# Kernel optimization log

Measured on AMD Instinct MI355X. Metric: run time of the kernel, lower is better.

Reference implementation:

```python
import jax, jax.numpy as jnp
import numpy as np

B, N, D = 2, 128, 128          # batch, nodes, dim
DE = 64                        # dim_edge_refinement
H, DH = 8, 32                  # heads, per-head dim
DI = H * DH                    # dim_inner = dim * dim_head = 256
DMI = 2 * DI                   # mlp_expansion_factor * dim_inner = 512
MD = 2                         # max_degree
S = 1 + 2 * MD                 # value/edge channel groups = 5
FFD = 512                      # int(2.0 * dim * 2) for EquivariantFeedForward


def _ln(x, g, eps=1e-5):
    mu = x.mean(-1, keepdims=True)
    var = ((x - mu) ** 2).mean(-1, keepdims=True)
    return (x - mu) / jnp.sqrt(var + eps) * g


def setup_inputs() -> dict:
    key = jax.random.key(0)
    ks = iter(jax.random.split(key, 64))
    def rn(shape, scale=1.0):
        return jax.random.normal(next(ks), shape, dtype=jnp.float32) * scale
    w = 0.05
    return dict(
        h=rn((B, N, D)), x1=rn((B, N, D, 3)), x2=rn((B, N, D, 5)),
        t_ij=rn((B, N, N, D)), r1=rn((B, N, N, 3)), r2=rn((B, N, N, 5)),
        g_i=jnp.ones((D,), jnp.float32), g_j=jnp.ones((D,), jnp.float32),
        Wq=rn((D, DI), w), Wk=rn((D, DI), w),
        Wv1=rn((D, DMI), w), bv1=jnp.zeros((DMI,), jnp.float32),
        Wv2=rn((DMI, S * DI), w), bv2=jnp.zeros((S * DI,), jnp.float32),
        Wp1=rn((D, DMI), w), bp1=jnp.zeros((DMI,), jnp.float32),
        Wp2=rn((DMI, S * DI), w), bp2=jnp.zeros((S * DI,), jnp.float32),
        Wek=rn((D, S * DI), w), Wev=rn((D, S * DI), w),
        Wcomb=rn((DI, D), w),
        Wqh=rn((D, DE), w), Wk1h=rn((D, DE), w), Wk2h=rn((D, DE), w),
        Wep=rn((2 * DE, D), w), Wres=rn((D, D), w),
        P1=rn((D, D), w), P2=rn((D, D), w),
        Wf1a=rn((2 * D, FFD), w), bf1a=jnp.zeros((FFD,), jnp.float32),
        Wf2a=rn((FFD, 2 * D), w), bf2a=jnp.zeros((2 * D,), jnp.float32),
        Wf1b=rn((2 * D, FFD), w), bf1b=jnp.zeros((FFD,), jnp.float32),
        Wf2b=rn((FFD, 2 * D), w), bf2b=jnp.zeros((2 * D,), jnp.float32),
    )


def reference(h, x1, x2, t_ij, r1, r2, g_i, g_j, Wq, Wk, Wv1, bv1, Wv2, bv2,
              Wp1, bp1, Wp2, bp2, Wek, Wev, Wcomb, Wqh, Wk1h, Wk2h, Wep, Wres,
              P1, P2, Wf1a, bf1a, Wf2a, bf2a, Wf1b, bf1b, Wf2b, bf2b):
    # ---- HierarchicalTensorRefinement: per-degree inner products -> edge refresh
    q1 = jnp.einsum('bndm,de->bnem', x1, Wqh)
    q2 = jnp.einsum('bndm,de->bnem', x2, Wqh)
    k1 = jnp.einsum('bndm,de->bnem', x1, Wk1h)
    k2 = jnp.einsum('bndm,de->bnem', x2, Wk2h)
    w_ij = jnp.concatenate([
        jnp.einsum('biem,bjem->bije', q1, k1),
        jnp.einsum('biem,bjem->bije', q2, k2)], axis=-1)       # [b,n,n,2*DE]
    t = w_ij @ Wep + t_ij @ Wres                                # [b,n,n,D]
    # ---- GeometryAwareTensorAttention
    hi = _ln(h, g_i)
    hj = _ln(h, g_j)
    q = (hi @ Wq).reshape(B, N, H, DH).transpose(0, 2, 1, 3)    # bhnd
    k = (hj @ Wk).reshape(B, N, H, DH).transpose(0, 2, 1, 3)
    v = (jax.nn.silu(hj @ Wv1 + bv1) @ Wv2 + bv2).reshape(B, N, S, H, DH).transpose(0, 3, 1, 2, 4)   # bhnsd
    pv = (jax.nn.silu(hj @ Wp1 + bp1) @ Wp2 + bp2).reshape(B, N, S, H, DH).transpose(0, 3, 1, 2, 4)
    ek = jax.nn.silu(t @ Wek).reshape(B, N, N, S, H, DH).transpose(0, 4, 1, 2, 3, 5)                  # bhijsd
    ev = (t @ Wev).reshape(B, N, N, S, H, DH).transpose(0, 4, 1, 2, 3, 5)
    sim_num = jnp.einsum('bhid,bhjd->bhij', q, k)
    sim_den = jnp.einsum('bhid,bhijsd->bhis', q, ek)            # edge-keyed denominator
    attn = sim_num[..., None] / sim_den[:, :, :, None, :]       # bhijs
    sea = attn[..., None] * v[:, :, None] + ev * pv[:, :, None]  # bhijsd
    out = sea.transpose(0, 2, 3, 4, 1, 5).reshape(B, N, N, S, H * DH) @ Wcomb  # [b,i,j,S,D]
    h_sc = out[..., 0, :]              # [b,i,j,D]
    r_sc = out[..., 1:1 + MD, :]       # [b,i,j,MD,D]
    x_sc = out[..., 1 + MD:, :]        # [b,i,j,MD,D]
    h2 = h + h_sc.sum(axis=2)
    x1a = jnp.einsum('bjdm,bijd->bidm', x1, x_sc[..., 0, :]) + jnp.einsum('bijm,bijd->bidm', r1, r_sc[..., 0, :])
    x2a = jnp.einsum('bjdm,bijd->bidm', x2, x_sc[..., 1, :]) + jnp.einsum('bijm,bijd->bidm', r2, r_sc[..., 1, :])
    # ---- EquivariantFeedForward (eq 13)
    def ff_branch(xl, P, W1, b1, W2, b2):
        proj = jnp.einsum('bndm,de->bnem', xl, P)
        inv = jnp.sqrt((proj ** 2).sum(-1) + 1e-12)             # invariant norm over m
        mo = jax.nn.silu(jnp.concatenate([h2, inv], -1) @ W1 + b1) @ W2 + b2
        m1, m2 = jnp.split(mo, 2, axis=-1)
        return m1, proj * m2[..., None]
    m1a, xr1 = ff_branch(x1a, P1, Wf1a, bf1a, Wf2a, bf2a)
    m1b, xr2 = ff_branch(x2a, P2, Wf1b, bf1b, Wf2b, bf2b)
    h3 = h2 + m1a + m1b
    x1f = x1a + xr1
    x2f = x2a + xr2
    # pack outputs: h [b,n,d,1] | x1 [b,n,d,3] | x2 [b,n,d,5] -> [b,n,d,9]
    return jnp.concatenate([h3[..., None], x1f, x2f], axis=-1)
```

## Files before the change

### kernel.cpp

```cpp
#include <hip/hip_runtime.h>
#include <math.h>

#define OFF_Q    0
#define OFF_K    65536
#define OFF_A1V  131072
#define OFF_A1P  262144
#define OFF_V    393216
#define OFF_PV   720896
#define OFF_VW   1048576
#define OFF_QK   2359296
#define OFF_T    2621440
#define OFF_DEN  6815744
#define OFF_ACC  6825984
#define OFF_WEVT 7940096
#define OFF_WCT  8022016
#define OFF_HI   8038400
#define OFF_HJ   8071168

typedef __bf16 bf16x8 __attribute__((ext_vector_type(8)));
typedef float  f32x4  __attribute__((ext_vector_type(4)));

__device__ __forceinline__ float silu_f(float x){
  return x / (1.0f + __expf(-x));
}
__device__ __forceinline__ unsigned short f2bf(float x){
  union{float f; unsigned u;} c; c.f = x;
  unsigned r = c.u + 0x7FFFu + ((c.u >> 16) & 1u);
  return (unsigned short)(r >> 16);
}
__device__ __forceinline__ unsigned packbf(float a, float b){
  return (unsigned)f2bf(a) | ((unsigned)f2bf(b) << 16);
}
__device__ __forceinline__ void swz_store(float* Abase, int k, int j, float v){
  *(float*)((char*)Abase + k*256 + ((((j>>2) ^ ((k>>2)&15))) << 4) + ((j&3)<<2)) = v;
}
__device__ __forceinline__ f32x4 swz_load4(const float* Abase, int k, int chunk){
  return *(const f32x4*)((const char*)Abase + k*256 + ((chunk ^ ((k>>2)&15)) << 4));
}

__global__ __launch_bounds__(128) void k0a_ln(
    const float* __restrict__ h, const float* __restrict__ g_i, const float* __restrict__ g_j,
    float* __restrict__ ws)
{
  __shared__ float red[2];
  const int r = blockIdx.x, tid = threadIdx.x;
  const int w = tid >> 6, l = tid & 63;
  const float hv = h[r*128 + tid];
  float s = hv;
  #pragma unroll
  for (int o = 1; o < 64; o <<= 1) s += __shfl_xor(s, o);
  if (l == 0) red[w] = s;
  __syncthreads();
  const float mu = (red[0] + red[1]) * (1.f/128.f);
  const float dv = hv - mu;
  float s2 = dv*dv;
  #pragma unroll
  for (int o = 1; o < 64; o <<= 1) s2 += __shfl_xor(s2, o);
  __syncthreads();
  if (l == 0) red[w] = s2;
  __syncthreads();
  const float rstd = 1.0f / sqrtf((red[0] + red[1])*(1.f/128.f) + 1e-5f);
  ws[OFF_HI + r*128 + tid] = dv * rstd * g_i[tid];
  ws[OFF_HJ + r*128 + tid] = dv * rstd * g_j[tid];
  if (tid < 40) ws[OFF_DEN + r*40 + tid] = 0.f;
}

__global__ __launch_bounds__(256) void k0b_qkv(
    const float* __restrict__ Wq, const float* __restrict__ Wk,
    const float* __restrict__ Wv1, const float* __restrict__ bv1,
    const float* __restrict__ Wp1, const float* __restrict__ bp1,
    float* __restrict__ ws)
{
  __shared__ float hrow[128];
  const int bid = blockIdx.x;
  const int row = bid / 6, ch = bid - 6*(bid/6);
  const int tid = threadIdx.x;
  if (tid < 128) hrow[tid] = ws[((ch == 0) ? OFF_HI : OFF_HJ) + row*128 + tid];
  __syncthreads();
  const float* W; int c; float bias = 0.f; bool act = false; float* dst; int wstride;
  switch(ch){
    case 0: W = Wq;  c = tid;      wstride = 256; dst = ws + OFF_Q   + row*256 + c; break;
    case 1: W = Wk;  c = tid;      wstride = 256; dst = ws + OFF_K   + row*256 + c; break;
    case 2: W = Wv1; c = tid;      wstride = 512; bias = bv1[c]; act = true; dst = ws + OFF_A1V + row*512 + c; break;
    case 3: W = Wv1; c = 256+tid;  wstride = 512; bias = bv1[c]; act = true; dst = ws + OFF_A1V + row*512 + c; break;
    case 4: W = Wp1; c = tid;      wstride = 512; bias = bp1[c]; act = true; dst = ws + OFF_A1P + row*512 + c; break;
    default:W = Wp1; c = 256+tid;  wstride = 512; bias = bp1[c]; act = true; dst = ws + OFF_A1P + row*512 + c; break;
  }
  float acc = bias;
  #pragma unroll 8
  for (int d = 0; d < 128; ++d) acc += hrow[d] * W[d*wstride + c];
  *dst = act ? silu_f(acc) : acc;
}

__global__ __launch_bounds__(256) void k0c_qk12(
    const float* __restrict__ x1, const float* __restrict__ x2,
    const float* __restrict__ Wqh, const float* __restrict__ Wk1h, const float* __restrict__ Wk2h,
    float* __restrict__ ws)
{
  __shared__ float x1r[384], x2r[640];
  const int row = blockIdx.x, tid = threadIdx.x;
  for (int idx = tid; idx < 384; idx += 256) x1r[idx] = x1[row*384 + idx];
  for (int idx = tid; idx < 640; idx += 256) x2r[idx] = x2[row*640 + idx];
  __syncthreads();
  for (int idx = tid; idx < 512; idx += 256){
    if (idx < 192){
      const int e = idx/3, m = idx - e*3;
      float qa = 0.f, ka = 0.f;
      #pragma unroll 8
      for (int d = 0; d < 128; ++d){
        const float xv = x1r[d*3 + m];
        qa += xv*Wqh[d*64 + e];
        ka += xv*Wk1h[d*64 + e];
      }
      ws[OFF_QK + row*1024 + idx] = qa;
      ws[OFF_QK + row*1024 + 512 + idx] = ka;
    } else {
      const int i2 = idx - 192;
      const int e = i2/5, m = i2 - e*5;
      float qa = 0.f, ka = 0.f;
      #pragma unroll 8
      for (int d = 0; d < 128; ++d){
        const float xv = x2r[d*5 + m];
        qa += xv*Wqh[d*64 + e];
        ka += xv*Wk2h[d*64 + e];
      }
      ws[OFF_QK + row*1024 + 192 + i2] = qa;
      ws[OFF_QK + row*1024 + 704 + i2] = ka;
    }
  }
}

__global__ __launch_bounds__(256) void k1_vp(
    const float* __restrict__ Wv2, const float* __restrict__ bv2,
    const float* __restrict__ Wp2, const float* __restrict__ bp2,
    float* __restrict__ ws)
{
  __shared__ float A[512][16];
  __shared__ float Bc[64][128];
  const int tid = threadIdx.x;
  const int rt = blockIdx.x & 31;
  const int ct = blockIdx.x >> 5;
  const int r0 = rt*16;
  const bool isP = (r0 >= 256);
  const int rbase = isP ? (r0 - 256) : r0;
  const float* __restrict__ src  = ws + (isP ? OFF_A1P : OFF_A1V);
  const float* __restrict__ W    = isP ? Wp2 : Wv2;
  const float* __restrict__ bias = isP ? bp2 : bv2;
  const int c0 = ct*128;
  for (int idx = tid; idx < 2048; idx += 256){
    const int rl = idx & 15;
    const int c4 = (idx >> 4) * 4;
    const float4 v = *(const float4*)&src[(rbase+rl)*512 + c4];
    A[c4+0][rl] = v.x; A[c4+1][rl] = v.y; A[c4+2][rl] = v.z; A[c4+3][rl] = v.w;
  }
  float acc[4][2] = {{0.f}};
  const int rg = tid & 3;
  const int cg = tid >> 2;
  for (int kc = 0; kc < 8; ++kc){
    __syncthreads();
    for (int idx = tid; idx < 2048; idx += 256){
      const int kl = idx >> 5;
      const int c4 = (idx & 31)*4;
      *(float4*)&Bc[kl][c4] = *(const float4*)&W[(kc*64+kl)*1280 + c0 + c4];
    }
    __syncthreads();
    #pragma unroll 8
    for (int k = 0; k < 64; ++k){
      const float4 a = *(const float4*)&A[kc*64+k][rg*4];
      const float b0 = Bc[k][cg*2], b1 = Bc[k][cg*2+1];
      acc[0][0] += a.x*b0; acc[0][1] += a.x*b1;
      acc[1][0] += a.y*b0; acc[1][1] += a.y*b1;
      acc[2][0] += a.z*b0; acc[2][1] += a.z*b1;
      acc[3][0] += a.w*b0; acc[3][1] += a.w*b1;
    }
  }
  float* __restrict__ dst = ws + (isP ? OFF_PV : OFF_V);
  for (int rr = 0; rr < 4; ++rr)
    for (int cc = 0; cc < 2; ++cc){
      const int c = c0 + cg*2 + cc;
      dst[(rbase + rg*4 + rr)*1280 + c] = acc[rr][cc] + bias[c];
    }
}

__global__ __launch_bounds__(256) void k2_vw(const float* __restrict__ Wcomb, float* __restrict__ ws)
{
  __shared__ float vr[1280];
  const int j = blockIdx.x, tid = threadIdx.x;
  for (int idx = tid; idx < 320; idx += 256)
    *(float4*)&vr[idx*4] = *(const float4*)&ws[OFF_V + j*1280 + idx*4];
  __syncthreads();
  const int d = tid & 127;
  for (int sh = tid >> 7; sh < 40; sh += 2){
    const int s = sh >> 3, hh = sh & 7;
    float a = 0.f;
    #pragma unroll 8
    for (int dh = 0; dh < 32; ++dh)
      a += vr[s*256 + hh*32 + dh] * Wcomb[(hh*32+dh)*128 + d];
    ws[OFF_VW + j*5120 + sh*128 + d] = a;
  }
}

__global__ __launch_bounds__(256) void k_cvt(
    const float* __restrict__ Wev, const float* __restrict__ Wcomb, float* __restrict__ ws)
{
  __shared__ float ld[16][256];
  const int tid = threadIdx.x;
  if (blockIdx.x < 80){
    const int c0 = blockIdx.x*16;
    for (int p = 0; p < 8; ++p){
      const int idx = tid + p*256;
      const int k = idx >> 4, cl = idx & 15;
      ld[cl][k] = Wev[k*1280 + c0 + cl];
    }
    __syncthreads();
    const int cl = tid >> 4, k8 = tid & 15;
    uint4 u;
    u.x = packbf(ld[cl][k8*8+0], ld[cl][k8*8+1]);
    u.y = packbf(ld[cl][k8*8+2], ld[cl][k8*8+3]);
    u.z = packbf(ld[cl][k8*8+4], ld[cl][k8*8+5]);
    u.w = packbf(ld[cl][k8*8+6], ld[cl][k8*8+7]);
    ((uint4*)(ws + OFF_WEVT))[(c0+cl)*16 + k8] = u;
  } else {
    const int c0 = (blockIdx.x - 80)*16;
    for (int p = 0; p < 16; ++p){
      const int idx = tid + p*256;
      const int k = idx >> 4, cl = idx & 15;
      ld[cl][k] = Wcomb[k*128 + c0 + cl];
    }
    __syncthreads();
    const int cl = tid >> 4, k8i = tid & 15;
    for (int pass = 0; pass < 2; ++pass){
      const int k8 = k8i + pass*16;
      uint4 u;
      u.x = packbf(ld[cl][k8*8+0], ld[cl][k8*8+1]);
      u.y = packbf(ld[cl][k8*8+2], ld[cl][k8*8+3]);
      u.z = packbf(ld[cl][k8*8+4], ld[cl][k8*8+5]);
      u.w = packbf(ld[cl][k8*8+6], ld[cl][k8*8+7]);
      ((uint4*)(ws + OFF_WCT))[(c0+cl)*32 + k8] = u;
    }
  }
}

__global__ __launch_bounds__(512, 2) void k3_t(
    const float* __restrict__ t_ij, const float* __restrict__ Wep, const float* __restrict__ Wres,
    float* __restrict__ ws)
{
  __shared__ float A[16384];
  __shared__ float qrow[512];
  float* kst = A + 8192;
  const int tid = threadIdx.x;
  const int bi = blockIdx.x >> 1;
  const int jt = blockIdx.x & 1;
  const int j0 = jt*64;
  const int b  = bi >> 7;
  if (tid < 128) *(float4*)&qrow[tid*4] = *(const float4*)&ws[OFF_QK + bi*1024 + tid*4];
  for (int jq = 0; jq < 4; ++jq){
    __syncthreads();
    for (int idx = tid; idx < 2048; idx += 512){
      const int jl = idx & 15;
      const int c4 = (idx >> 4)*4;
      const float4 v = *(const float4*)&ws[OFF_QK + (b*128 + j0 + jq*16 + jl)*1024 + 512 + c4];
      kst[(c4+0)*16 + jl] = v.x; kst[(c4+1)*16 + jl] = v.y;
      kst[(c4+2)*16 + jl] = v.z; kst[(c4+3)*16 + jl] = v.w;
    }
    __syncthreads();
    for (int idx = tid; idx < 2048; idx += 512){
      const int jl = idx & 15;
      const int e  = idx >> 4;
      float acc = 0.f;
      if (e < 64){
        #pragma unroll
        for (int m = 0; m < 3; ++m) acc += qrow[e*3+m] * kst[(e*3+m)*16 + jl];
      } else {
        const int e2 = e - 64;
        #pragma unroll
        for (int m = 0; m < 5; ++m) acc += qrow[192 + e2*5+m] * kst[(192 + e2*5+m)*16 + jl];
      }
      swz_store(A, e, jq*16 + jl, acc);
    }
  }
  __syncthreads();
  for (int idx = tid; idx < 2048; idx += 512){
    const int jl = idx >> 5;
    const int d4 = (idx & 31)*4;
    const float4 v = *(const float4*)&t_ij[(bi*128 + j0 + jl)*128 + d4];
    swz_store(A, 128+d4+0, jl, v.x);
    swz_store(A, 128+d4+1, jl, v.y);
    swz_store(A, 128+d4+2, jl, v.z);
    swz_store(A, 128+d4+3, jl, v.w);
  }
  __syncthreads();
  const int jg = tid >> 5;
  const int cg = tid & 31;
  f32x4 acc[4] = {{0,0,0,0},{0,0,0,0},{0,0,0,0},{0,0,0,0}};
  {
    const float* Wp = Wep + cg*4;
    f32x4 wv = *(const f32x4*)Wp;
    for (int k = 0; k < 127; ++k){
      const f32x4 wn = *(const f32x4*)(Wp + (k+1)*128);
      const f32x4 av = swz_load4(A, k, jg);
      acc[0] += wv*av[0]; acc[1] += wv*av[1]; acc[2] += wv*av[2]; acc[3] += wv*av[3];
      wv = wn;
    }
    const f32x4 av = swz_load4(A, 127, jg);
    acc[0] += wv*av[0]; acc[1] += wv*av[1]; acc[2] += wv*av[2]; acc[3] += wv*av[3];
  }
  {
    const float* Wp = Wres + cg*4;
    f32x4 wv = *(const f32x4*)Wp;
    for (int k = 0; k < 127; ++k){
      const f32x4 wn = *(const f32x4*)(Wp + (k+1)*128);
      const f32x4 av = swz_load4(A, 128+k, jg);
      acc[0] += wv*av[0]; acc[1] += wv*av[1]; acc[2] += wv*av[2]; acc[3] += wv*av[3];
      wv = wn;
    }
    const f32x4 av = swz_load4(A, 255, jg);
    acc[0] += wv*av[0]; acc[1] += wv*av[1]; acc[2] += wv*av[2]; acc[3] += wv*av[3];
  }
  #pragma unroll
  for (int jj = 0; jj < 4; ++jj)
    *(f32x4*)&ws[OFF_T + (bi*128 + j0 + jg*4 + jj)*128 + cg*4] = acc[jj];
}

__global__ __launch_bounds__(256) void k4_den(
    const float* __restrict__ Wek, float* __restrict__ ws)
{
  __shared__ float tl[8192];
  __shared__ float colsum[8][128];
  __shared__ float den40[40];
  const int tid = threadIdx.x;
  const int bid = blockIdx.x;
  const int bi = bid / 20;
  const int rem = bid - bi*20;
  const int jh = rem & 1;
  const int cq = rem >> 1;
  const int j0 = jh*64;
  for (int idx = tid; idx < 2048; idx += 256){
    const int j = idx >> 5;
    const int d4 = (idx & 31)*4;
    const float4 v = *(const float4*)&ws[OFF_T + (bi*128 + j0 + j)*128 + d4];
    swz_store(tl, d4+0, j, v.x);
    swz_store(tl, d4+1, j, v.y);
    swz_store(tl, d4+2, j, v.z);
    swz_store(tl, d4+3, j, v.w);
  }
  if (tid < 40) den40[tid] = 0.f;
  __syncthreads();
  const int w = tid >> 5;
  const int lane = tid & 31;
  const float* wekp = Wek + cq*128 + lane*4;
  f32x4 acc[8];
  #pragma unroll
  for (int i = 0; i < 8; ++i) acc[i] = (f32x4){0,0,0,0};
  f32x4 wv = *(const f32x4*)wekp;
  for (int k = 0; k < 127; ++k){
    const f32x4 wn = *(const f32x4*)(wekp + (k+1)*1280);
    #pragma unroll
    for (int q = 0; q < 2; ++q){
      const f32x4 tv = swz_load4(tl, k, w*2 + q);
      acc[q*4+0] += wv*tv[0]; acc[q*4+1] += wv*tv[1];
      acc[q*4+2] += wv*tv[2]; acc[q*4+3] += wv*tv[3];
    }
    wv = wn;
  }
  #pragma unroll
  for (int q = 0; q < 2; ++q){
    const f32x4 tv = swz_load4(tl, 127, w*2 + q);
    acc[q*4+0] += wv*tv[0]; acc[q*4+1] += wv*tv[1];
    acc[q*4+2] += wv*tv[2]; acc[q*4+3] += wv*tv[3];
  }
  f32x4 cs = {0,0,0,0};
  #pragma unroll
  for (int i = 0; i < 8; ++i){
    #pragma unroll
    for (int cc = 0; cc < 4; ++cc) cs[cc] += silu_f(acc[i][cc]);
  }
  *(f32x4*)&colsum[w][lane*4] = cs;
  __syncthreads();
  if (tid < 128){
    const int c = tid;
    const float jsum = colsum[0][c] + colsum[1][c] + colsum[2][c] + colsum[3][c]
                     + colsum[4][c] + colsum[5][c] + colsum[6][c] + colsum[7][c];
    const int col = cq*128 + c;
    const int s  = col >> 8;
    const int hd = col & 255;
    atomicAdd(&den40[(hd>>5)*5 + s], jsum * ws[OFF_Q + bi*256 + hd]);
  }
  __syncthreads();
  if (tid < 40 && den40[tid] != 0.f)
    atomicAdd(&ws[OFF_DEN + bi*40 + tid], den40[tid]);
}

__global__ __launch_bounds__(512) void k5_pass2(
    const float* __restrict__ x1, const float* __restrict__ x2,
    const float* __restrict__ r1, const float* __restrict__ r2,
    float* __restrict__ ws)
{
  __shared__ unsigned short epB[2][4096];
  __shared__ float num[8][64];
  __shared__ float acc17[17*128];
  __shared__ float ql[256];
  __shared__ float rdenl[40];

  const int tid  = threadIdx.x;
  const int lane = tid & 63;
  const int w    = tid >> 6;
  const int wm   = w & 3;
  const int wn   = w >> 2;
  const int l15  = lane & 15;
  const int kq   = lane >> 4;

  const int bi = blockIdx.x >> 1;
  const int jh = blockIdx.x & 1;
  const int j0 = jh*64;
  const int b  = bi >> 7;

  if (tid < 64) *(float4*)&ql[tid*4] = *(const float4*)&ws[OFF_Q + bi*256 + tid*4];
  if (tid < 40) rdenl[tid] = 1.0f / ws[OFF_DEN + bi*40 + tid];
  for (int idx = tid; idx < 17*128; idx += 512) acc17[idx] = 0.f;

  const int jA = wm*16 + l15;
  union { bf16x8 v; uint4 q; } afu[4];
  #pragma unroll
  for (int ks = 0; ks < 4; ++ks){
    const float* tp = &ws[OFF_T + (bi*128 + j0 + jA)*128 + ks*32 + kq*8];
    const float4 t0 = *(const float4*)tp;
    const float4 t1 = *(const float4*)(tp + 4);
    afu[ks].q.x = packbf(t0.x, t0.y);
    afu[ks].q.y = packbf(t0.z, t0.w);
    afu[ks].q.z = packbf(t1.x, t1.y);
    afu[ks].q.w = packbf(t1.z, t1.w);
  }
  __syncthreads();

  {
    const int hh = tid >> 6, jl = tid & 63;
    const float* krow = &ws[OFF_K + (b*128 + j0 + jl)*256 + hh*32];
    float a = 0.f;
    #pragma unroll
    for (int dh = 0; dh < 32; ++dh) a += ql[hh*32+dh]*krow[dh];
    num[hh][jl] = a;
  }

  const __bf16* wevt = (const __bf16*)(ws + OFF_WEVT);
  const __bf16* wct  = (const __bf16*)(ws + OFF_WCT);

  int pb = 0;
  for (int s = 0; s < 5; ++s){
    f32x4 o0 = {0,0,0,0}, o1 = {0,0,0,0}, o2 = {0,0,0,0}, o3 = {0,0,0,0};
    for (int ch4 = 0; ch4 < 4; ++ch4){
      const int cb = s*256 + ch4*64;
      f32x4 ev0 = {0,0,0,0}, ev1 = {0,0,0,0};
      {
        const int c0l = wn*32 + l15;
        const int c1l = c0l + 16;
        #pragma unroll
        for (int ks = 0; ks < 4; ++ks){
          const bf16x8 b0 = *(const bf16x8*)(wevt + (cb + c0l)*128 + ks*32 + kq*8);
          const bf16x8 b1 = *(const bf16x8*)(wevt + (cb + c1l)*128 + ks*32 + kq*8);
          ev0 = __builtin_amdgcn_mfma_f32_16x16x32_bf16(afu[ks].v, b0, ev0, 0, 0, 0);
          ev1 = __builtin_amdgcn_mfma_f32_16x16x32_bf16(afu[ks].v, b1, ev1, 0, 0, 0);
        }
      }
      #pragma unroll
      for (int nt = 0; nt < 2; ++nt){
        const int cl = wn*32 + nt*16 + l15;
        const int cglob = cb + cl;
        #pragma unroll
        for (int r = 0; r < 4; ++r){
          const int jl = wm*16 + kq*4 + r;
          const float pvv = ws[OFF_PV + (b*128 + j0 + jl)*1280 + cglob];
          const float evv = (nt == 0) ? ev0[r] : ev1[r];
          *(unsigned short*)((char*)epB[pb] + jl*128 + ((cl*2) ^ ((jl&7)<<4))) = f2bf(evv * pvv);
        }
      }
      __syncthreads();
      #pragma unroll
      for (int ks = 0; ks < 2; ++ks){
        const bf16x8 a = *(const bf16x8*)((const char*)epB[pb] + jA*128 + ((ks*64 + kq*16) ^ ((jA&7)<<4)));
        #pragma unroll
        for (int nt = 0; nt < 4; ++nt){
          const int dl = wn*64 + nt*16 + l15;
          const bf16x8 bb = *(const bf16x8*)(wct + dl*256 + ch4*64 + ks*32 + kq*8);
          if      (nt == 0) o0 = __builtin_amdgcn_mfma_f32_16x16x32_bf16(a, bb, o0, 0, 0, 0);
          else if (nt == 1) o1 = __builtin_amdgcn_mfma_f32_16x16x32_bf16(a, bb, o1, 0, 0, 0);
          else if (nt == 2) o2 = __builtin_amdgcn_mfma_f32_16x16x32_bf16(a, bb, o2, 0, 0, 0);
          else              o3 = __builtin_amdgcn_mfma_f32_16x16x32_bf16(a, bb, o3, 0, 0, 0);
        }
      }
      pb ^= 1;
    }
    #pragma unroll
    for (int r = 0; r < 4; ++r){
      const int jl = wm*16 + kq*4 + r;
      const float* vwbase = ws + OFF_VW + (b*128 + j0 + jl)*5120 + s*1024 + wn*64 + l15;
      #pragma unroll
      for (int hh = 0; hh < 8; ++hh){
        const float at = num[hh][jl] * rdenl[hh*5 + s];
        const float* vp = vwbase + hh*128;
        o0[r] += at * vp[0];
        o1[r] += at * vp[16];
        o2[r] += at * vp[32];
        o3[r] += at * vp[48];
      }
    }
    if (s == 0){
      #pragma unroll
      for (int nt = 0; nt < 4; ++nt){
        const f32x4 oo = (nt==0)?o0:(nt==1)?o1:(nt==2)?o2:o3;
        float p = oo[0] + oo[1] + oo[2] + oo[3];
        p += __shfl_xor(p, 16);
        p += __shfl_xor(p, 32);
        if (lane < 16) atomicAdd(&acc17[wn*64 + nt*16 + lane], p);
      }
    } else if (s <= 2){
      const int M = (s == 1) ? 3 : 5;
      const int slot0 = (s == 1) ? 1 : 4;
      const float* rw = (s == 1) ? r1 : r2;
      for (int m = 0; m < M; ++m){
        float wj[4];
        #pragma unroll
        for (int r = 0; r < 4; ++r)
          wj[r] = rw[(bi*128 + j0 + wm*16 + kq*4 + r)*M + m];
        #pragma unroll
        for (int nt = 0; nt < 4; ++nt){
          const f32x4 oo = (nt==0)?o0:(nt==1)?o1:(nt==2)?o2:o3;
          float p = wj[0]*oo[0] + wj[1]*oo[1] + wj[2]*oo[2] + wj[3]*oo[3];
          p += __shfl_xor(p, 16);
          p += __shfl_xor(p, 32);
          if (lane < 16) atomicAdd(&acc17[(slot0+m)*128 + wn*64 + nt*16 + lane], p);
        }
      }
    } else {
      const int M = (s == 3) ? 3 : 5;
      const int slot0 = (s == 3) ? 9 : 12;
      const float* xw = (s == 3) ? x1 : x2;
      for (int m = 0; m < M; ++m){
        #pragma unroll
        for (int nt = 0; nt < 4; ++nt){
          const int d = wn*64 + nt*16 + l15;
          const f32x4 oo = (nt==0)?o0:(nt==1)?o1:(nt==2)?o2:o3;
          float p = 0.f;
          #pragma unroll
          for (int r = 0; r < 4; ++r)
            p += xw[((b*128 + j0 + wm*16 + kq*4 + r)*128 + d)*M + m] * oo[r];
          p += __shfl_xor(p, 16);
          p += __shfl_xor(p, 32);
          if (lane < 16) atomicAdd(&acc17[(slot0+m)*128 + d], p);
        }
      }
    }
  }
  __syncthreads();
  for (int idx = tid; idx < 2176; idx += 512)
    ws[OFF_ACC + (bi*2 + jh)*2176 + idx] = acc17[idx];
}

__global__ __launch_bounds__(256) void k6_tail(
    const float* __restrict__ h,
    const float* __restrict__ P1, const float* __restrict__ P2,
    const float* __restrict__ Wf1a, const float* __restrict__ bf1a,
    const float* __restrict__ Wf2a, const float* __restrict__ bf2a,
    const float* __restrict__ Wf1b, const float* __restrict__ bf1b,
    const float* __restrict__ Wf2b, const float* __restrict__ bf2b,
    const float* __restrict__ ws, float* __restrict__ out)
{
  __shared__ float a17[2176];
  __shared__ float h2s[128];
  __shared__ float x1a[384], x2a[640];
  __shared__ float pj1[384], pj2[640];
  __shared__ float inv1[128], inv2[128];
  __shared__ float za[512], zb[512];
  __shared__ float m1a[128], m2a[128], m1b[128], m2b[128];
  const int tid = threadIdx.x;
  const int row = blockIdx.x;
  for (int idx = tid; idx < 2176; idx += 256)
    a17[idx] = ws[OFF_ACC + (row*2)*2176 + idx] + ws[OFF_ACC + (row*2+1)*2176 + idx];
  __syncthreads();
  if (tid < 128) h2s[tid] = h[row*128 + tid] + a17[tid];
  for (int idx = tid; idx < 384; idx += 256){
    const int d = idx/3, m = idx - d*3;
    x1a[idx] = a17[(1+m)*128 + d] + a17[(9+m)*128 + d];
  }
  for (int idx = tid; idx < 640; idx += 256){
    const int d = idx/5, m = idx - d*5;
    x2a[idx] = a17[(4+m)*128 + d] + a17[(12+m)*128 + d];
  }
  __syncthreads();
  if (tid < 128){
    const int e = tid;
    float pa[3] = {0.f,0.f,0.f};
    for (int d = 0; d < 128; ++d){
      const float p = P1[d*128 + e];
      pa[0] += x1a[d*3+0]*p;
      pa[1] += x1a[d*3+1]*p;
      pa[2] += x1a[d*3+2]*p;
    }
    pj1[e*3+0] = pa[0]; pj1[e*3+1] = pa[1]; pj1[e*3+2] = pa[2];
    inv1[e] = sqrtf(pa[0]*pa[0] + pa[1]*pa[1] + pa[2]*pa[2] + 1e-12f);
  } else {
    const int e = tid - 128;
    float pa[5] = {0.f,0.f,0.f,0.f,0.f};
    for (int d = 0; d < 128; ++d){
      const float p = P2[d*128 + e];
      pa[0] += x2a[d*5+0]*p;
      pa[1] += x2a[d*5+1]*p;
      pa[2] += x2a[d*5+2]*p;
      pa[3] += x2a[d*5+3]*p;
      pa[4] += x2a[d*5+4]*p;
    }
    #pragma unroll
    for (int m = 0; m < 5; ++m) pj2[e*5+m] = pa[m];
    inv2[e] = sqrtf(pa[0]*pa[0]+pa[1]*pa[1]+pa[2]*pa[2]+pa[3]*pa[3]+pa[4]*pa[4] + 1e-12f);
  }
  __syncthreads();
  for (int it = 0; it < 2; ++it){
    const int f = tid + it*256;
    float av = bf1a[f], bv_ = bf1b[f];
    #pragma unroll 4
    for (int k = 0; k < 128; ++k){
      av  += h2s[k]*Wf1a[k*512 + f];
      bv_ += h2s[k]*Wf1b[k*512 + f];
    }
    #pragma unroll 4
    for (int k = 0; k < 128; ++k){
      av  += inv1[k]*Wf1a[(128+k)*512 + f];
      bv_ += inv2[k]*Wf1b[(128+k)*512 + f];
    }
    za[f] = silu_f(av); zb[f] = silu_f(bv_);
  }
  __syncthreads();
  {
    const int g = tid;
    float am = bf2a[g], bm = bf2b[g];
    #pragma unroll 4
    for (int f = 0; f < 512; ++f){
      am += za[f]*Wf2a[f*256 + g];
      bm += zb[f]*Wf2b[f*256 + g];
    }
    if (g < 128){ m1a[g] = am; m1b[g] = bm; }
    else        { m2a[g-128] = am; m2b[g-128] = bm; }
  }
  __syncthreads();
  if (tid < 128){
    const int d = tid;
    const int ob = (row*128 + d)*9;
    out[ob+0] = h2s[d] + m1a[d] + m1b[d];
    #pragma unroll
    for (int m = 0; m < 3; ++m)
      out[ob+1+m] = x1a[d*3+m] + pj1[d*3+m]*m2a[d];
    #pragma unroll
    for (int m = 0; m < 5; ++m)
      out[ob+4+m] = x2a[d*5+m] + pj2[d*5+m]*m2b[d];
  }
}

extern "C" void kernel_launch(void* const* d_in, const int* in_sizes, int n_in,
                              void* d_out, int out_size, void* d_ws, size_t ws_size,
                              hipStream_t stream)
{
  (void)in_sizes; (void)n_in; (void)out_size; (void)ws_size;
  const float* h    = (const float*)d_in[0];
  const float* x1   = (const float*)d_in[1];
  const float* x2   = (const float*)d_in[2];
  const float* t_ij = (const float*)d_in[3];
  const float* r1   = (const float*)d_in[4];
  const float* r2   = (const float*)d_in[5];
  const float* g_i  = (const float*)d_in[6];
  const float* g_j  = (const float*)d_in[7];
  const float* Wq   = (const float*)d_in[8];
  const float* Wk   = (const float*)d_in[9];
  const float* Wv1  = (const float*)d_in[10];
  const float* bv1  = (const float*)d_in[11];
  const float* Wv2  = (const float*)d_in[12];
  const float* bv2  = (const float*)d_in[13];
  const float* Wp1  = (const float*)d_in[14];
  const float* bp1  = (const float*)d_in[15];
  const float* Wp2  = (const float*)d_in[16];
  const float* bp2  = (const float*)d_in[17];
  const float* Wek  = (const float*)d_in[18];
  const float* Wev  = (const float*)d_in[19];
  const float* Wcomb= (const float*)d_in[20];
  const float* Wqh  = (const float*)d_in[21];
  const float* Wk1h = (const float*)d_in[22];
  const float* Wk2h = (const float*)d_in[23];
  const float* Wep  = (const float*)d_in[24];
  const float* Wres = (const float*)d_in[25];
  const float* P1   = (const float*)d_in[26];
  const float* P2   = (const float*)d_in[27];
  const float* Wf1a = (const float*)d_in[28];
  const float* bf1a = (const float*)d_in[29];
  const float* Wf2a = (const float*)d_in[30];
  const float* bf2a = (const float*)d_in[31];
  const float* Wf1b = (const float*)d_in[32];
  const float* bf1b = (const float*)d_in[33];
  const float* Wf2b = (const float*)d_in[34];
  const float* bf2b = (const float*)d_in[35];
  float* ws  = (float*)d_ws;
  float* out = (float*)d_out;

  k0a_ln <<<dim3(256),  dim3(128), 0, stream>>>(h, g_i, g_j, ws);
  k0b_qkv<<<dim3(1536), dim3(256), 0, stream>>>(Wq, Wk, Wv1, bv1, Wp1, bp1, ws);
  k0c_qk12<<<dim3(256), dim3(256), 0, stream>>>(x1, x2, Wqh, Wk1h, Wk2h, ws);
  k1_vp  <<<dim3(320),  dim3(256), 0, stream>>>(Wv2, bv2, Wp2, bp2, ws);
  k2_vw  <<<dim3(256),  dim3(256), 0, stream>>>(Wcomb, ws);
  k_cvt  <<<dim3(88),   dim3(256), 0, stream>>>(Wev, Wcomb, ws);
  k3_t   <<<dim3(512),  dim3(512), 0, stream>>>(t_ij, Wep, Wres, ws);
  k4_den <<<dim3(5120), dim3(256), 0, stream>>>(Wek, ws);
  k5_pass2<<<dim3(512), dim3(512), 0, stream>>>(x1, x2, r1, r2, ws);
  k6_tail<<<dim3(256),  dim3(256), 0, stream>>>(h, P1, P2, Wf1a, bf1a, Wf2a, bf2a, Wf1b, bf1b, Wf2b, bf2b, ws, out);
}
```

Measured before the change: 717.5 us.

## Split k5_pass2 across channel groups into separate blocks for more parallelism

The k5 pass now launches one block per (row, j-half, channel group s) with 256 threads, instead of one 512-thread block looping over all five groups. Each wave owns 16 rows and all 128 output columns, so it holds eight MFMA accumulators instead of four. This raises the block count fivefold to fill the GPU better and shrinks shared memory to only the slots for one group. In exchange, each block redoes the T-tile bf16 conversion and the q·k numerator, and per-thread register pressure goes up.

```diff
diff --git a/kernel.cpp b/kernel.cpp
--- a/kernel.cpp
+++ b/kernel.cpp
@@ -391,35 +391,39 @@
     atomicAdd(&ws[OFF_DEN + bi*40 + tid], den40[tid]);
 }
 
-__global__ __launch_bounds__(512) void k5_pass2(
+__global__ __launch_bounds__(256) void k5_pass2(
     const float* __restrict__ x1, const float* __restrict__ x2,
     const float* __restrict__ r1, const float* __restrict__ r2,
     float* __restrict__ ws)
 {
   __shared__ unsigned short epB[2][4096];
   __shared__ float num[8][64];
-  __shared__ float acc17[17*128];
+  __shared__ float accS[5*128];
   __shared__ float ql[256];
-  __shared__ float rdenl[40];
+  __shared__ float rden8[8];
 
   const int tid  = threadIdx.x;
   const int lane = tid & 63;
   const int w    = tid >> 6;
-  const int wm   = w & 3;
-  const int wn   = w >> 2;
   const int l15  = lane & 15;
   const int kq   = lane >> 4;
 
-  const int bi = blockIdx.x >> 1;
-  const int jh = blockIdx.x & 1;
-  const int j0 = jh*64;
-  const int b  = bi >> 7;
-
-  if (tid < 64) *(float4*)&ql[tid*4] = *(const float4*)&ws[OFF_Q + bi*256 + tid*4];
-  if (tid < 40) rdenl[tid] = 1.0f / ws[OFF_DEN + bi*40 + tid];
-  for (int idx = tid; idx < 17*128; idx += 512) acc17[idx] = 0.f;
-
-  const int jA = wm*16 + l15;
+  const int bid = blockIdx.x;
+  const int bi  = bid / 10;
+  const int rem = bid - bi*10;
+  const int jh  = rem & 1;
+  const int s   = rem >> 1;
+  const int j0  = jh*64;
+  const int b   = bi >> 7;
+
+  const int M     = (s == 0) ? 1 : ((s == 1 || s == 3) ? 3 : 5);
+  const int slot0 = (s == 0) ? 0 : (s == 1) ? 1 : (s == 2) ? 4 : (s == 3) ? 9 : 12;
+
+  ql[tid] = ws[OFF_Q + bi*256 + tid];
+  if (tid < 8) rden8[tid] = 1.0f / ws[OFF_DEN + bi*40 + tid*5 + s];
+  for (int idx = tid; idx < M*128; idx += 256) accS[idx] = 0.f;
+
+  const int jA = w*16 + l15;
   union { bf16x8 v; uint4 q; } afu[4];
   #pragma unroll
   for (int ks = 0; ks < 4; ++ks){
@@ -433,8 +437,8 @@
   }
   __syncthreads();
 
-  {
-    const int hh = tid >> 6, jl = tid & 63;
+  for (int idx = tid; idx < 512; idx += 256){
+    const int hh = idx >> 6, jl = idx & 63;
     const float* krow = &ws[OFF_K + (b*128 + j0 + jl)*256 + hh*32];
     float a = 0.f;
     #pragma unroll
@@ -445,115 +449,120 @@
   const __bf16* wevt = (const __bf16*)(ws + OFF_WEVT);
   const __bf16* wct  = (const __bf16*)(ws + OFF_WCT);
 
+  f32x4 o0={0,0,0,0},o1={0,0,0,0},o2={0,0,0,0},o3={0,0,0,0},
+        o4={0,0,0,0},o5={0,0,0,0},o6={0,0,0,0},o7={0,0,0,0};
   int pb = 0;
-  for (int s = 0; s < 5; ++s){
-    f32x4 o0 = {0,0,0,0}, o1 = {0,0,0,0}, o2 = {0,0,0,0}, o3 = {0,0,0,0};
-    for (int ch4 = 0; ch4 < 4; ++ch4){
-      const int cb = s*256 + ch4*64;
-      f32x4 ev0 = {0,0,0,0}, ev1 = {0,0,0,0};
-      {
-        const int c0l = wn*32 + l15;
-        const int c1l = c0l + 16;
-        #pragma unroll
-        for (int ks = 0; ks < 4; ++ks){
-          const bf16x8 b0 = *(const bf16x8*)(wevt + (cb + c0l)*128 + ks*32 + kq*8);
-          const bf16x8 b1 = *(const bf16x8*)(wevt + (cb + c1l)*128 + ks*32 + kq*8);
-          ev0 = __builtin_amdgcn_mfma_f32_16x16x32_bf16(afu[ks].v, b0, ev0, 0, 0, 0);
-          ev1 = __builtin_amdgcn_mfma_f32_16x16x32_bf16(afu[ks].v, b1, ev1, 0, 0, 0);
-        }
+  for (int ch4 = 0; ch4 < 4; ++ch4){
+    const int cb = s*256 + ch4*64;
+    f32x4 ev0={0,0,0,0},ev1={0,0,0,0},ev2={0,0,0,0},ev3={0,0,0,0};
+    #pragma unroll
+    for (int ks = 0; ks < 4; ++ks){
+      const __bf16* bp = wevt + (cb + l15)*128 + ks*32 + kq*8;
+      const bf16x8 b0 = *(const bf16x8*)(bp);
+      const bf16x8 b1 = *(const bf16x8*)(bp + 16*128);
+      const bf16x8 b2 = *(const bf16x8*)(bp + 32*128);
+      const bf16x8 b3 = *(const bf16x8*)(bp + 48*128);
+      ev0 = __builtin_amdgcn_mfma_f32_16x16x32_bf16(afu[ks].v, b0, ev0, 0, 0, 0);
+      ev1 = __builtin_amdgcn_mfma_f32_16x16x32_bf16(afu[ks].v, b1, ev1, 0, 0, 0);
+      ev2 = __builtin_amdgcn_mfma_f32_16x16x32_bf16(afu[ks].v, b2, ev2, 0, 0, 0);
+      ev3 = __builtin_amdgcn_mfma_f32_16x16x32_bf16(afu[ks].v, b3, ev3, 0, 0, 0);
+    }
+    #pragma unroll
+    for (int nt = 0; nt < 4; ++nt){
+      const int cl = nt*16 + l15;
+      const int cglob = cb + cl;
+      const f32x4 evv = (nt==0)?ev0:(nt==1)?ev1:(nt==2)?ev2:ev3;
+      #pragma unroll
+      for (int r = 0; r < 4; ++r){
+        const int jl = w*16 + kq*4 + r;
+        const float pvv = ws[OFF_PV + (b*128 + j0 + jl)*1280 + cglob];
+        *(unsigned short*)((char*)epB[pb] + jl*128 + ((cl*2) ^ ((jl&7)<<4))) = f2bf(evv[r] * pvv);
       }
+    }
+    __syncthreads();
+    #pragma unroll
+    for (int ks = 0; ks < 2; ++ks){
+      const bf16x8 a = *(const bf16x8*)((const char*)epB[pb] + jA*128 + ((ks*64 + kq*16) ^ ((jA&7)<<4)));
       #pragma unroll
-      for (int nt = 0; nt < 2; ++nt){
-        const int cl = wn*32 + nt*16 + l15;
-        const int cglob = cb + cl;
-        #pragma unroll
-        for (int r = 0; r < 4; ++r){
-          const int jl = wm*16 + kq*4 + r;
-          const float pvv = ws[OFF_PV + (b*128 + j0 + jl)*1280 + cglob];
-          const float evv = (nt == 0) ? ev0[r] : ev1[r];
-          *(unsigned short*)((char*)epB[pb] + jl*128 + ((cl*2) ^ ((jl&7)<<4))) = f2bf(evv * pvv);
-        }
+      for (int nt = 0; nt < 8; ++nt){
+        const int dl = nt*16 + l15;
+        const bf16x8 bb = *(const bf16x8*)(wct + dl*256 + ch4*64 + ks*32 + kq*8);
+        if      (nt == 0) o0 = __builtin_amdgcn_mfma_f32_16x16x32_bf16(a, bb, o0, 0, 0, 0);
+        else if (nt == 1) o1 = __builtin_amdgcn_mfma_f32_16x16x32_bf16(a, bb, o1, 0, 0, 0);
+        else if (nt == 2) o2 = __builtin_amdgcn_mfma_f32_16x16x32_bf16(a, bb, o2, 0, 0, 0);
+        else if (nt == 3) o3 = __builtin_amdgcn_mfma_f32_16x16x32_bf16(a, bb, o3, 0, 0, 0);
+        else if (nt == 4) o4 = __builtin_amdgcn_mfma_f32_16x16x32_bf16(a, bb, o4, 0, 0, 0);
+        else if (nt == 5) o5 = __builtin_amdgcn_mfma_f32_16x16x32_bf16(a, bb, o5, 0, 0, 0);
+        else if (nt == 6) o6 = __builtin_amdgcn_mfma_f32_16x16x32_bf16(a, bb, o6, 0, 0, 0);
+        else              o7 = __builtin_amdgcn_mfma_f32_16x16x32_bf16(a, bb, o7, 0, 0, 0);
       }
-      __syncthreads();
+    }
+    pb ^= 1;
+  }
+  #pragma unroll
+  for (int r = 0; r < 4; ++r){
+    const int jl = w*16 + kq*4 + r;
+    const float* vwbase = ws + OFF_VW + (b*128 + j0 + jl)*5120 + s*1024 + l15;
+    #pragma unroll
+    for (int hh = 0; hh < 8; ++hh){
+      const float at = num[hh][jl] * rden8[hh];
+      const float* vp = vwbase + hh*128;
+      o0[r] += at * vp[0];
+      o1[r] += at * vp[16];
+      o2[r] += at * vp[32];
+      o3[r] += at * vp[48];
+      o4[r] += at * vp[64];
+      o5[r] += at * vp[80];
+      o6[r] += at * vp[96];
+      o7[r] += at * vp[112];
+    }
+  }
+  if (s == 0){
+    #pragma unroll
+    for (int nt = 0; nt < 8; ++nt){
+      const f32x4 oo = (nt==0)?o0:(nt==1)?o1:(nt==2)?o2:(nt==3)?o3:(nt==4)?o4:(nt==5)?o5:(nt==6)?o6:o7;
+      float p = oo[0] + oo[1] + oo[2] + oo[3];
+      p += __shfl_xor(p, 16);
+      p += __shfl_xor(p, 32);
+      if (l15 == lane) ;
+      if (lane < 16) atomicAdd(&accS[nt*16 + lane], p);
+    }
+  } else if (s <= 2){
+    const float* rw = (s == 1) ? r1 : r2;
+    for (int m = 0; m < M; ++m){
+      float wj[4];
       #pragma unroll
-      for (int ks = 0; ks < 2; ++ks){
-        const bf16x8 a = *(const bf16x8*)((const char*)epB[pb] + jA*128 + ((ks*64 + kq*16) ^ ((jA&7)<<4)));
-        #pragma unroll
-        for (int nt = 0; nt < 4; ++nt){
-          const int dl = wn*64 + nt*16 + l15;
-          const bf16x8 bb = *(const bf16x8*)(wct + dl*256 + ch4*64 + ks*32 + kq*8);
-          if      (nt == 0) o0 = __builtin_amdgcn_mfma_f32_16x16x32_bf16(a, bb, o0, 0, 0, 0);
-          else if (nt == 1) o1 = __builtin_amdgcn_mfma_f32_16x16x32_bf16(a, bb, o1, 0, 0, 0);
-          else if (nt == 2) o2 = __builtin_amdgcn_mfma_f32_16x16x32_bf16(a, bb, o2, 0, 0, 0);
-          else              o3 = __builtin_amdgcn_mfma_f32_16x16x32_bf16(a, bb, o3, 0, 0, 0);
-        }
-      }
-      pb ^= 1;
-    }
-    #pragma unroll
-    for (int r = 0; r < 4; ++r){
-      const int jl = wm*16 + kq*4 + r;
-      const float* vwbase = ws + OFF_VW + (b*128 + j0 + jl)*5120 + s*1024 + wn*64 + l15;
+      for (int r = 0; r < 4; ++r)
+        wj[r] = rw[(bi*128 + j0 + w*16 + kq*4 + r)*M + m];
       #pragma unroll
-      for (int hh = 0; hh < 8; ++hh){
-        const float at = num[hh][jl] * rdenl[hh*5 + s];
-        const float* vp = vwbase + hh*128;
-        o0[r] += at * vp[0];
-        o1[r] += at * vp[16];
-        o2[r] += at * vp[32];
-        o3[r] += at * vp[48];
-      }
-    }
-    if (s == 0){
-      #pragma unroll
-      for (int nt = 0; nt < 4; ++nt){
-        const f32x4 oo = (nt==0)?o0:(nt==1)?o1:(nt==2)?o2:o3;
-        float p = oo[0] + oo[1] + oo[2] + oo[3];
+      for (int nt = 0; nt < 8; ++nt){
+        const f32x4 oo = (nt==0)?o0:(nt==1)?o1:(nt==2)?o2:(nt==3)?o3:(nt==4)?o4:(nt==5)?o5:(nt==6)?o6:o7;
+        float p = wj[0]*oo[0] + wj[1]*oo[1] + wj[2]*oo[2] + wj[3]*oo[3];
         p += __shfl_xor(p, 16);
         p += __shfl_xor(p, 32);
-        if (lane < 16) atomicAdd(&acc17[wn*64 + nt*16 + lane], p);
+        if (lane < 16) atomicAdd(&accS[m*128 + nt*16 + lane], p);
       }
-    } else if (s <= 2){
-      const int M = (s == 1) ? 3 : 5;
-      const int slot0 = (s == 1) ? 1 : 4;
-      const float* rw = (s == 1) ? r1 : r2;
-      for (int m = 0; m < M; ++m){
-        float wj[4];
+    }
+  } else {
+    const float* xw = (s == 3) ? x1 : x2;
+    for (int m = 0; m < M; ++m){
+      #pragma unroll
+      for (int nt = 0; nt < 8; ++nt){
+        const int d = nt*16 + l15;
+        const f32x4 oo = (nt==0)?o0:(nt==1)?o1:(nt==2)?o2:(nt==3)?o3:(nt==4)?o4:(nt==5)?o5:(nt==6)?o6:o7;
+        float p = 0.f;
         #pragma unroll
         for (int r = 0; r < 4; ++r)
-          wj[r] = rw[(bi*128 + j0 + wm*16 + kq*4 + r)*M + m];
-        #pragma unroll
-        for (int nt = 0; nt < 4; ++nt){
-          const f32x4 oo = (nt==0)?o0:(nt==1)?o1:(nt==2)?o2:o3;
-          float p = wj[0]*oo[0] + wj[1]*oo[1] + wj[2]*oo[2] + wj[3]*oo[3];
-          p += __shfl_xor(p, 16);
-          p += __shfl_xor(p, 32);
-          if (lane < 16) atomicAdd(&acc17[(slot0+m)*128 + wn*64 + nt*16 + lane], p);
-        }
+          p += xw[((b*128 + j0 + w*16 + kq*4 + r)*128 + d)*M + m] * oo[r];
+        p += __shfl_xor(p, 16);
+        p += __shfl_xor(p, 32);
+        if (lane < 16) atomicAdd(&accS[m*128 + d], p);
       }
-    } else {
-      const int M = (s == 3) ? 3 : 5;
-      const int slot0 = (s == 3) ? 9 : 12;
-      const float* xw = (s == 3) ? x1 : x2;
-      for (int m = 0; m < M; ++m){
-        #pragma unroll
-        for (int nt = 0; nt < 4; ++nt){
-          const int d = wn*64 + nt*16 + l15;
-          const f32x4 oo = (nt==0)?o0:(nt==1)?o1:(nt==2)?o2:o3;
-          float p = 0.f;
-          #pragma unroll
-          for (int r = 0; r < 4; ++r)
-            p += xw[((b*128 + j0 + wm*16 + kq*4 + r)*128 + d)*M + m] * oo[r];
-          p += __shfl_xor(p, 16);
-          p += __shfl_xor(p, 32);
-          if (lane < 16) atomicAdd(&acc17[(slot0+m)*128 + d], p);
-        }
-      }
-    }
-  }
-  __syncthreads();
-  for (int idx = tid; idx < 2176; idx += 512)
-    ws[OFF_ACC + (bi*2 + jh)*2176 + idx] = acc17[idx];
+    }
+  }
+  __syncthreads();
+  for (int idx = tid; idx < M*128; idx += 256)
+    ws[OFF_ACC + (bi*2 + jh)*2176 + slot0*128 + idx] = accS[idx];
 }
 
 __global__ __launch_bounds__(256) void k6_tail(
@@ -707,6 +716,6 @@
   k_cvt  <<<dim3(88),   dim3(256), 0, stream>>>(Wev, Wcomb, ws);
   k3_t   <<<dim3(512),  dim3(512), 0, stream>>>(t_ij, Wep, Wres, ws);
   k4_den <<<dim3(5120), dim3(256), 0, stream>>>(Wek, ws);
-  k5_pass2<<<dim3(512), dim3(512), 0, stream>>>(x1, x2, r1, r2, ws);
+  k5_pass2<<<dim3(2560),dim3(256), 0, stream>>>(x1, x2, r1, r2, ws);
   k6_tail<<<dim3(256),  dim3(256), 0, stream>>>(h, P1, P2, Wf1a, bf1a, Wf2a, bf2a, Wf1b, bf1b, Wf2b, bf2b, ws, out);
 }
```

Measured after the change: 763.8 us. +6.5%, slower.
